# Kernel tuning notes

Measured on AMD Instinct MI355X. Metric: run time of the kernel, lower is better.

Reference implementation:

```python
import jax, jax.numpy as jnp
import numpy as np

B, T, E, H = 256, 256, 384, 64  # batch, seq (== block_size), embed_dim, head_size

def setup_inputs() -> dict:
    key = jax.random.key(0)
    kx, kq, kk, kv = jax.random.split(key, 4)
    scale = 1.0 / np.sqrt(E)
    return {
        "x": jax.random.normal(kx, (B, T, E), dtype=jnp.float32),
        "Wq": jax.random.normal(kq, (E, H), dtype=jnp.float32) * scale,
        "Wk": jax.random.normal(kk, (E, H), dtype=jnp.float32) * scale,
        "Wv": jax.random.normal(kv, (E, H), dtype=jnp.float32) * scale,
    }

def reference(x, Wq, Wk, Wv):
    # Linear projections (bias-free), faithful to nn.Linear(embed_dim, head_size, bias=False)
    q = jnp.einsum("bte,eh->bth", x, Wq)
    k = jnp.einsum("bte,eh->bth", x, Wk)
    v = jnp.einsum("bte,eh->bth", x, Wv)
    # Scaled QK^T with causal mask, softmax, weighted sum.
    # Dropout is identity in eval mode (reference is deterministic).
    wei = jnp.einsum("bth,bsh->bts", q, k) * (H ** -0.5)  # [B, T, T]
    causal = jnp.tril(jnp.ones((T, T), dtype=bool))
    wei = jnp.where(causal, wei, -jnp.inf)
    wei = jax.nn.softmax(wei, axis=-1)
    out = jnp.einsum("bts,bsh->bth", wei, v)  # [B, T, H]
    return out
```

## Files before the change

kernel.cpp:

```cpp
#include <hip/hip_runtime.h>
#include <hip/hip_bf16.h>

typedef __attribute__((ext_vector_type(8))) short short8;
typedef __attribute__((ext_vector_type(4))) float f32x4;
typedef __attribute__((ext_vector_type(16))) float f32x16;

#define MFMA16(a, b, c) __builtin_amdgcn_mfma_f32_16x16x32_bf16((a), (b), (c), 0, 0, 0)
#define MFMA32(a, b, c) __builtin_amdgcn_mfma_f32_32x32x16_bf16((a), (b), (c), 0, 0, 0)

__device__ __forceinline__ unsigned short f2bf(float f) {
  union { float f; unsigned int u; } v; v.f = f;
  unsigned int u = v.u;
  unsigned int r = u + 0x7FFFu + ((u >> 16) & 1u);
  return (unsigned short)(r >> 16);
}

__device__ __forceinline__ unsigned int f2bf2(float a, float b) {
  __hip_bfloat162 h2 = __float22bfloat162_rn(make_float2(a, b));
  union { __hip_bfloat162 h; unsigned int u; } cv; cv.h = h2;
  return cv.u;
}

__global__ void wconv_kernel(const float* __restrict__ Wq, const float* __restrict__ Wk,
                             const float* __restrict__ Wv, unsigned short* __restrict__ W3t) {
  int j = blockIdx.x * 128 + threadIdx.x;
  int s2 = j / 384;
  int r = j - s2 * 384;
  int c = r >> 6, l = r & 63;
  int col = 32 * c + (l & 31);
  int k = 16 * s2 + 8 * (l >> 5);
  const float* src = (col < 64) ? Wq : ((col < 128) ? Wk : Wv);
  int sc = col & 63;
  float e[8];
#pragma unroll
  for (int i = 0; i < 8; ++i) e[i] = src[(k + i) * 64 + sc];
  uint4 u;
  u.x = f2bf2(e[0], e[1]); u.y = f2bf2(e[2], e[3]);
  u.z = f2bf2(e[4], e[5]); u.w = f2bf2(e[6], e[7]);
  *(uint4*)&W3t[j * 8] = u;
}

__global__ __launch_bounds__(512) void fused_kernel(
    const float* __restrict__ x, const unsigned short* __restrict__ W3t,
    float* __restrict__ out) {
  extern __shared__ unsigned short sm[];
  unsigned short* Ql = sm;
  unsigned short* Kl = sm + 18432;
  unsigned short* Vl = sm + 36864;

  const int tid = threadIdx.x;
  const int w = tid >> 6, lane = tid & 63, g = lane >> 4, q = lane & 15;
  const int l31 = lane & 31, h = lane >> 5;
  const int b = blockIdx.x;
  const float* xb = x + (long)b * 98304;

#pragma unroll
  for (int i = 0; i < 18; ++i) {
    int idx = tid + i * 512;
    *(uint4*)&sm[idx * 8] = *(const uint4*)&W3t[idx * 8];
  }

  f32x16 acc[6];
#pragma unroll
  for (int j = 0; j < 6; ++j)
#pragma unroll
    for (int r = 0; r < 16; ++r) acc[j][r] = 0.f;

  const float* xrow = xb + (32 * w + l31) * 384 + 8 * h;
  float4 c0 = *(const float4*)&xrow[0];
  float4 c1 = *(const float4*)&xrow[4];
  float4 c2 = *(const float4*)&xrow[16];
  float4 c3 = *(const float4*)&xrow[20];

  __syncthreads();

#pragma unroll
  for (int ks = 0; ks < 12; ++ks) {
    float4 n0, n1, n2, n3;
    if (ks < 11) {
      n0 = *(const float4*)&xrow[32 * (ks + 1)];
      n1 = *(const float4*)&xrow[32 * (ks + 1) + 4];
      n2 = *(const float4*)&xrow[32 * (ks + 1) + 16];
      n3 = *(const float4*)&xrow[32 * (ks + 1) + 20];
    }
    uint4 a0u, a1u;
    a0u.x = f2bf2(c0.x, c0.y); a0u.y = f2bf2(c0.z, c0.w);
    a0u.z = f2bf2(c1.x, c1.y); a0u.w = f2bf2(c1.z, c1.w);
    a1u.x = f2bf2(c2.x, c2.y); a1u.y = f2bf2(c2.z, c2.w);
    a1u.z = f2bf2(c3.x, c3.y); a1u.w = f2bf2(c3.z, c3.w);
    union { uint4 u; short8 s8; } av0, av1;
    av0.u = a0u; av1.u = a1u;
    const unsigned short* base = sm + (2 * ks) * 3072 + lane * 8;
#pragma unroll
    for (int ct = 0; ct < 6; ++ct) {
      short8 b0 = *(const short8*)&base[ct * 512];
      acc[ct] = MFMA32(av0.s8, b0, acc[ct]);
      short8 b1 = *(const short8*)&base[3072 + ct * 512];
      acc[ct] = MFMA32(av1.s8, b1, acc[ct]);
    }
    if (ks < 11) { c0 = n0; c1 = n1; c2 = n2; c3 = n3; }
  }
  __syncthreads();

#pragma unroll
  for (int ct = 0; ct < 6; ++ct) {
    const int C = 32 * ct + l31;
    if (ct < 2) {
#pragma unroll
      for (int r = 0; r < 16; ++r) {
        int row = 32 * w + (r & 3) + 8 * (r >> 2) + 4 * h;
        Ql[row * 72 + C] = f2bf(acc[ct][r]);
      }
    } else if (ct < 4) {
      const int cc = C - 64;
#pragma unroll
      for (int r = 0; r < 16; ++r) {
        int row = 32 * w + (r & 3) + 8 * (r >> 2) + 4 * h;
        Kl[row * 72 + cc] = f2bf(acc[ct][r]);
      }
    } else {
      const int hh = C - 128;
#pragma unroll
      for (int rq = 0; rq < 4; ++rq) {
        int mb = 32 * w + 8 * rq + 4 * h;
        uint2 pk;
        pk.x = f2bf2(acc[ct][4 * rq + 0], acc[ct][4 * rq + 1]);
        pk.y = f2bf2(acc[ct][4 * rq + 2], acc[ct][4 * rq + 3]);
        *(uint2*)&Vl[hh * 264 + mb] = pk;
      }
    }
  }
  __syncthreads();

  unsigned short* Pb = sm + 53760 + w * 640;
  const float SCL = 0.125f * 1.4426950408889634f;
  const f32x4 zf = {0.f, 0.f, 0.f, 0.f};

#pragma unroll
  for (int ti = 0; ti < 2; ++ti) {
    const int t = ti ? (15 - w) : w;

    short8 aq0 = *(const short8*)&Ql[(16 * t + q) * 72 + g * 8];
    short8 aq1 = *(const short8*)&Ql[(16 * t + q) * 72 + 32 + g * 8];

    f32x4 o[4];
#pragma unroll
    for (int ct = 0; ct < 4; ++ct) o[ct] = zf;
    float m = -1e30f;
    float lsum = 0.f;

    const int KS = (t >> 1) + 1;
    for (int ks = 0; ks < KS; ++ks) {
      const int j0 = 2 * ks, j1 = 2 * ks + 1;
      const bool has1 = (j1 <= t);
      short8 ka0 = *(const short8*)&Kl[(16 * j0 + q) * 72 + g * 8];
      short8 ka1 = *(const short8*)&Kl[(16 * j0 + q) * 72 + 32 + g * 8];
      f32x4 s0 = MFMA16(ka0, aq0, zf);
      s0 = MFMA16(ka1, aq1, s0);
      f32x4 s1 = zf;
      if (has1) {
        short8 kb0 = *(const short8*)&Kl[(16 * j1 + q) * 72 + g * 8];
        short8 kb1 = *(const short8*)&Kl[(16 * j1 + q) * 72 + 32 + g * 8];
        s1 = MFMA16(kb0, aq0, zf);
        s1 = MFMA16(kb1, aq1, s1);
      }
      float v[8];
#pragma unroll
      for (int jr = 0; jr < 4; ++jr) {
        float aa = s0[jr] * SCL;
        if (j0 == t && 4 * g + jr > q) aa = -1e30f;
        v[jr] = aa;
        float cc = has1 ? s1[jr] * SCL : -1e30f;
        if (has1 && j1 == t && 4 * g + jr > q) cc = -1e30f;
        v[4 + jr] = cc;
      }
      float mloc = fmaxf(fmaxf(fmaxf(v[0], v[1]), fmaxf(v[2], v[3])),
                         fmaxf(fmaxf(v[4], v[5]), fmaxf(v[6], v[7])));
      mloc = fmaxf(mloc, __shfl_xor(mloc, 16));
      mloc = fmaxf(mloc, __shfl_xor(mloc, 32));
      float mnew = fmaxf(m, mloc);
      float f = exp2f(m - mnew);
      m = mnew;
      float p[8];
      float ls = 0.f;
#pragma unroll
      for (int i = 0; i < 8; ++i) { p[i] = exp2f(v[i] - mnew); ls += p[i]; }
      lsum = lsum * f + ls;
#pragma unroll
      for (int jr = 0; jr < 4; ++jr) {
        float fr = __shfl(f, 4 * g + jr);
        o[0][jr] *= fr; o[1][jr] *= fr; o[2][jr] *= fr; o[3][jr] *= fr;
      }
      uint2 pa; pa.x = f2bf2(p[0], p[1]); pa.y = f2bf2(p[2], p[3]);
      *(uint2*)&Pb[q * 40 + 4 * g] = pa;
      uint2 pc; pc.x = f2bf2(p[4], p[5]); pc.y = f2bf2(p[6], p[7]);
      *(uint2*)&Pb[q * 40 + 16 + 4 * g] = pc;
      short8 ap = *(const short8*)&Pb[q * 40 + g * 8];
#pragma unroll
      for (int ct = 0; ct < 4; ++ct) {
        short8 bv = *(const short8*)&Vl[(16 * ct + q) * 264 + ks * 32 + g * 8];
        o[ct] = MFMA16(ap, bv, o[ct]);
      }
    }

    lsum += __shfl_xor(lsum, 16);
    lsum += __shfl_xor(lsum, 32);
    float linv[4];
#pragma unroll
    for (int jr = 0; jr < 4; ++jr) linv[jr] = 1.0f / __shfl(lsum, 4 * g + jr);

    const long rowbase = (long)b * 256 + 16 * t;
#pragma unroll
    for (int jr = 0; jr < 4; ++jr) {
#pragma unroll
      for (int ct = 0; ct < 4; ++ct) {
        out[(rowbase + 4 * g + jr) * 64 + 16 * ct + q] = o[ct][jr] * linv[jr];
      }
    }
  }
}

extern "C" void kernel_launch(void* const* d_in, const int* in_sizes, int n_in,
                              void* d_out, int out_size, void* d_ws, size_t ws_size,
                              hipStream_t stream) {
  const float* x  = (const float*)d_in[0];
  const float* Wq = (const float*)d_in[1];
  const float* Wk = (const float*)d_in[2];
  const float* Wv = (const float*)d_in[3];
  float* out = (float*)d_out;

  unsigned short* W3t = (unsigned short*)d_ws;

  hipFuncSetAttribute((const void*)fused_kernel,
                      hipFuncAttributeMaxDynamicSharedMemorySize, 147456);

  wconv_kernel<<<72, 128, 0, stream>>>(Wq, Wk, Wv, W3t);
  fused_kernel<<<256, 512, 147456, stream>>>(x, W3t, out);
}
```

Measured before the change: 39.48 us.

## Split fused projection+attention into separate projection and attention kernels

```diff
diff --git a/kernel.cpp b/kernel.cpp
--- a/kernel.cpp
+++ b/kernel.cpp
@@ -40,25 +40,15 @@
   *(uint4*)&W3t[j * 8] = u;
 }
 
-__global__ __launch_bounds__(512) void fused_kernel(
+__global__ __launch_bounds__(256) void proj_kernel(
     const float* __restrict__ x, const unsigned short* __restrict__ W3t,
-    float* __restrict__ out) {
-  extern __shared__ unsigned short sm[];
-  unsigned short* Ql = sm;
-  unsigned short* Kl = sm + 18432;
-  unsigned short* Vl = sm + 36864;
-
+    unsigned short* __restrict__ Qg, unsigned short* __restrict__ Kg,
+    unsigned short* __restrict__ Vtg) {
+  __shared__ unsigned short wl[2][6144];
   const int tid = threadIdx.x;
-  const int w = tid >> 6, lane = tid & 63, g = lane >> 4, q = lane & 15;
+  const int w = tid >> 6, lane = tid & 63;
   const int l31 = lane & 31, h = lane >> 5;
-  const int b = blockIdx.x;
-  const float* xb = x + (long)b * 98304;
-
-#pragma unroll
-  for (int i = 0; i < 18; ++i) {
-    int idx = tid + i * 512;
-    *(uint4*)&sm[idx * 8] = *(const uint4*)&W3t[idx * 8];
-  }
+  const long m0 = (long)blockIdx.x * 128;
 
   f32x16 acc[6];
 #pragma unroll
@@ -66,31 +56,37 @@
 #pragma unroll
     for (int r = 0; r < 16; ++r) acc[j][r] = 0.f;
 
-  const float* xrow = xb + (32 * w + l31) * 384 + 8 * h;
-  float4 c0 = *(const float4*)&xrow[0];
-  float4 c1 = *(const float4*)&xrow[4];
-  float4 c2 = *(const float4*)&xrow[16];
-  float4 c3 = *(const float4*)&xrow[20];
-
-  __syncthreads();
-
-#pragma unroll
-  for (int ks = 0; ks < 12; ++ks) {
-    float4 n0, n1, n2, n3;
-    if (ks < 11) {
-      n0 = *(const float4*)&xrow[32 * (ks + 1)];
-      n1 = *(const float4*)&xrow[32 * (ks + 1) + 4];
-      n2 = *(const float4*)&xrow[32 * (ks + 1) + 16];
-      n3 = *(const float4*)&xrow[32 * (ks + 1) + 20];
-    }
+  const float* xrow = x + (m0 + 32 * w + l31) * 384 + 8 * h;
+
+  float4 xsA[4], xsB[4];
+  uint4 wregA[3], wregB[3];
+
+  auto LX = [&](float4* d, int s) {
+    const float* p = xrow + 32 * s;
+    d[0] = *(const float4*)&p[0];
+    d[1] = *(const float4*)&p[4];
+    d[2] = *(const float4*)&p[16];
+    d[3] = *(const float4*)&p[20];
+  };
+  auto LW = [&](uint4* d, int s) {
+    d[0] = *(const uint4*)&W3t[((long)s * 768 + tid) * 8];
+    d[1] = *(const uint4*)&W3t[((long)s * 768 + tid + 256) * 8];
+    d[2] = *(const uint4*)&W3t[((long)s * 768 + tid + 512) * 8];
+  };
+  auto WW = [&](unsigned short* buf, const uint4* r) {
+    *(uint4*)&buf[tid * 8] = r[0];
+    *(uint4*)&buf[(tid + 256) * 8] = r[1];
+    *(uint4*)&buf[(tid + 512) * 8] = r[2];
+  };
+  auto COMPUTE = [&](const unsigned short* wb, const float4* c) {
     uint4 a0u, a1u;
-    a0u.x = f2bf2(c0.x, c0.y); a0u.y = f2bf2(c0.z, c0.w);
-    a0u.z = f2bf2(c1.x, c1.y); a0u.w = f2bf2(c1.z, c1.w);
-    a1u.x = f2bf2(c2.x, c2.y); a1u.y = f2bf2(c2.z, c2.w);
-    a1u.z = f2bf2(c3.x, c3.y); a1u.w = f2bf2(c3.z, c3.w);
+    a0u.x = f2bf2(c[0].x, c[0].y); a0u.y = f2bf2(c[0].z, c[0].w);
+    a0u.z = f2bf2(c[1].x, c[1].y); a0u.w = f2bf2(c[1].z, c[1].w);
+    a1u.x = f2bf2(c[2].x, c[2].y); a1u.y = f2bf2(c[2].z, c[2].w);
+    a1u.z = f2bf2(c[3].x, c[3].y); a1u.w = f2bf2(c[3].z, c[3].w);
     union { uint4 u; short8 s8; } av0, av1;
     av0.u = a0u; av1.u = a1u;
-    const unsigned short* base = sm + (2 * ks) * 3072 + lane * 8;
+    const unsigned short* base = wb + lane * 8;
 #pragma unroll
     for (int ct = 0; ct < 6; ++ct) {
       short8 b0 = *(const short8*)&base[ct * 512];
@@ -98,9 +94,26 @@
       short8 b1 = *(const short8*)&base[3072 + ct * 512];
       acc[ct] = MFMA32(av1.s8, b1, acc[ct]);
     }
-    if (ks < 11) { c0 = n0; c1 = n1; c2 = n2; c3 = n3; }
-  }
+  };
+
+  LX(xsA, 0); LW(wregA, 0);
+  WW(wl[0], wregA);
+  LX(xsB, 1); LW(wregB, 1);
   __syncthreads();
+
+#pragma unroll
+  for (int kp = 0; kp < 6; ++kp) {
+    COMPUTE(wl[0], xsA);
+    if (kp < 5) { LX(xsA, 2 * kp + 2); LW(wregA, 2 * kp + 2); }
+    WW(wl[1], wregB);
+    __syncthreads();
+    COMPUTE(wl[1], xsB);
+    if (kp < 5) {
+      LX(xsB, 2 * kp + 3); LW(wregB, 2 * kp + 3);
+      WW(wl[0], wregA);
+    }
+    __syncthreads();
+  }
 
 #pragma unroll
   for (int ct = 0; ct < 6; ++ct) {
@@ -108,31 +121,58 @@
     if (ct < 2) {
 #pragma unroll
       for (int r = 0; r < 16; ++r) {
-        int row = 32 * w + (r & 3) + 8 * (r >> 2) + 4 * h;
-        Ql[row * 72 + C] = f2bf(acc[ct][r]);
+        long row = m0 + 32 * w + (r & 3) + 8 * (r >> 2) + 4 * h;
+        Qg[row * 64 + C] = f2bf(acc[ct][r]);
       }
     } else if (ct < 4) {
       const int cc = C - 64;
 #pragma unroll
       for (int r = 0; r < 16; ++r) {
-        int row = 32 * w + (r & 3) + 8 * (r >> 2) + 4 * h;
-        Kl[row * 72 + cc] = f2bf(acc[ct][r]);
+        long row = m0 + 32 * w + (r & 3) + 8 * (r >> 2) + 4 * h;
+        Kg[row * 64 + cc] = f2bf(acc[ct][r]);
       }
     } else {
       const int hh = C - 128;
+      const long bb = m0 >> 8;
 #pragma unroll
       for (int rq = 0; rq < 4; ++rq) {
-        int mb = 32 * w + 8 * rq + 4 * h;
+        int tok = (int)(m0 & 255) + 32 * w + 8 * rq + 4 * h;
         uint2 pk;
         pk.x = f2bf2(acc[ct][4 * rq + 0], acc[ct][4 * rq + 1]);
         pk.y = f2bf2(acc[ct][4 * rq + 2], acc[ct][4 * rq + 3]);
-        *(uint2*)&Vl[hh * 264 + mb] = pk;
-      }
-    }
+        *(uint2*)&Vtg[(bb * 64 + hh) * 256 + tok] = pk;
+      }
+    }
+  }
+}
+
+__global__ __launch_bounds__(512) void attn_kernel(
+    const unsigned short* __restrict__ Qg, const unsigned short* __restrict__ Kg,
+    const unsigned short* __restrict__ Vtg, float* __restrict__ out) {
+  extern __shared__ unsigned short sm[];
+  unsigned short* Kl = sm;
+  unsigned short* Vl = sm + 18432;
+  const int tid = threadIdx.x;
+  const int w = tid >> 6, lane = tid & 63, g = lane >> 4, q = lane & 15;
+  const int b = blockIdx.x;
+  const unsigned short* Kgb = Kg + (long)b * 16384;
+  const unsigned short* Vgb = Vtg + (long)b * 16384;
+
+#pragma unroll
+  for (int it = 0; it < 4; ++it) {
+    int i = tid + it * 512;
+    int tok = i >> 3, k0 = (i & 7) * 8;
+    *(uint4*)&Kl[tok * 72 + k0] = *(const uint4*)&Kgb[tok * 64 + k0];
+  }
+#pragma unroll
+  for (int it = 0; it < 4; ++it) {
+    int i = tid + it * 512;
+    int hh = i >> 5, t0 = (i & 31) * 8;
+    *(uint4*)&Vl[hh * 264 + t0] = *(const uint4*)&Vgb[hh * 256 + t0];
   }
   __syncthreads();
 
-  unsigned short* Pb = sm + 53760 + w * 640;
+  unsigned short* Pb = sm + 35328 + w * 640;
   const float SCL = 0.125f * 1.4426950408889634f;
   const f32x4 zf = {0.f, 0.f, 0.f, 0.f};
 
@@ -140,8 +180,9 @@
   for (int ti = 0; ti < 2; ++ti) {
     const int t = ti ? (15 - w) : w;
 
-    short8 aq0 = *(const short8*)&Ql[(16 * t + q) * 72 + g * 8];
-    short8 aq1 = *(const short8*)&Ql[(16 * t + q) * 72 + 32 + g * 8];
+    const unsigned short* Qrow = Qg + ((long)b * 256 + 16 * t + q) * 64;
+    short8 aq0 = *(const short8*)&Qrow[g * 8];
+    short8 aq1 = *(const short8*)&Qrow[32 + g * 8];
 
     f32x4 o[4];
 #pragma unroll
@@ -229,11 +270,16 @@
   const float* Wv = (const float*)d_in[3];
   float* out = (float*)d_out;
 
-  unsigned short* W3t = (unsigned short*)d_ws;
-
-  hipFuncSetAttribute((const void*)fused_kernel,
-                      hipFuncAttributeMaxDynamicSharedMemorySize, 147456);
+  char* ws = (char*)d_ws;
+  unsigned short* W3t = (unsigned short*)ws;
+  unsigned short* Qg  = (unsigned short*)(ws + 147456);
+  unsigned short* Kg  = (unsigned short*)(ws + 147456 + 8388608);
+  unsigned short* Vtg = (unsigned short*)(ws + 147456 + 16777216);
+
+  hipFuncSetAttribute((const void*)attn_kernel,
+                      hipFuncAttributeMaxDynamicSharedMemorySize, 80896);
 
   wconv_kernel<<<72, 128, 0, stream>>>(Wq, Wk, Wv, W3t);
-  fused_kernel<<<256, 512, 147456, stream>>>(x, W3t, out);
-}
+  proj_kernel<<<512, 256, 0, stream>>>(x, W3t, Qg, Kg, Vtg);
+  attn_kernel<<<256, 512, 80896, stream>>>(Qg, Kg, Vtg, out);
+}
```

Result: slower. 68.64 us (+73.9%).
